# Optimization experiments

Hardware: AMD Instinct MI355X
Metric: run time of the kernel (lower is better)

The kernel has to match this reference:

```python
import jax, jax.numpy as jnp
import numpy as np

B, T, H, LATENT, P = 64, 256, 1024, 256, 128


def _lstm_layer(x, h0, c0, Wih, Whh, bih, bhh):
    """PyTorch-convention single-direction LSTM layer.
    x: (B,T,Din); returns hidden sequence (B,T,H). Gate order: i,f,g,o."""
    # Precompute the input contribution for all timesteps in one big GEMM.
    xg = jnp.einsum('btd,gd->btg', x, Wih) + bih + bhh  # (B,T,4H)

    def step(carry, xg_t):
        h, c = carry
        gates = xg_t + h @ Whh.T  # (B,4H)
        i, f, g, o = jnp.split(gates, 4, axis=-1)
        c = jax.nn.sigmoid(f) * c + jax.nn.sigmoid(i) * jnp.tanh(g)
        h = jax.nn.sigmoid(o) * jnp.tanh(c)
        return (h, c), h

    (_, _), hs = jax.lax.scan(step, (h0, c0), jnp.swapaxes(xg, 0, 1))
    return jnp.swapaxes(hs, 0, 1)  # (B,T,H)


def setup_inputs() -> dict:
    key = jax.random.key(0)
    ks = jax.random.split(key, 8)
    s = lambda fan_in: 1.0 / np.sqrt(fan_in)
    return {
        'z': jax.random.normal(ks[0], (B, LATENT), jnp.float32),
        'target_seq': jax.random.uniform(ks[1], (B, T, P), jnp.float32),
        'fc_init_w': jax.random.normal(ks[2], (H, LATENT), jnp.float32) * s(LATENT),
        'fc_init_b': jnp.zeros((H,), jnp.float32),
        'start_token': jax.random.normal(ks[3], (1, 1, P), jnp.float32) * 0.1,
        'W_ih_l0': jax.random.normal(ks[4], (4 * H, P), jnp.float32) * s(P),
        'W_hh_l0': jax.random.normal(ks[5], (4 * H, H), jnp.float32) * s(H),
        'b_ih_l0': jnp.zeros((4 * H,), jnp.float32),
        'b_hh_l0': jnp.zeros((4 * H,), jnp.float32),
        'W_ih_l1': jax.random.normal(ks[6], (4 * H, H), jnp.float32) * s(H),
        'W_hh_l1': jax.random.normal(ks[7], (4 * H, H), jnp.float32) * s(H),
        'b_ih_l1': jnp.zeros((4 * H,), jnp.float32),
        'b_hh_l1': jnp.zeros((4 * H,), jnp.float32),
        'out_w': jax.random.normal(jax.random.fold_in(key, 99), (P, H), jnp.float32) * s(H),
        'out_b': jnp.zeros((P,), jnp.float32),
    }


def reference(z, target_seq, fc_init_w, fc_init_b, start_token,
              W_ih_l0, W_hh_l0, b_ih_l0, b_hh_l0,
              W_ih_l1, W_hh_l1, b_ih_l1, b_hh_l1,
              out_w, out_b):
    # h0 = fc_init(z), shared across both LSTM layers (repeat over num_layers).
    h0 = z @ fc_init_w.T + fc_init_b  # (B,H)
    c0 = jnp.zeros_like(h0)
    # Full teacher forcing (teacher_forcing_ratio=1.0): input at step t is
    # target_seq[:, t-1]; step 0 uses the learned start token. Dropout is in
    # eval mode (identity).
    x_in = jnp.concatenate(
        [jnp.broadcast_to(start_token, (z.shape[0], 1, start_token.shape[-1])),
         target_seq[:, :-1, :]], axis=1)  # (B,T,P)
    h1 = _lstm_layer(x_in, h0, c0, W_ih_l0, W_hh_l0, b_ih_l0, b_hh_l0)
    h2 = _lstm_layer(h1, h0, c0, W_ih_l1, W_hh_l1, b_ih_l1, b_hh_l1)
    return jax.nn.sigmoid(jnp.einsum('bth,ph->btp', h2, out_w) + out_b)  # (B,T,P)
```

## Files before the change

kernel.cpp:

```cpp
#include <hip/hip_runtime.h>
#include <hip/hip_bf16.h>
#include <stdint.h>

typedef __attribute__((ext_vector_type(8))) short short8;
typedef __attribute__((ext_vector_type(4))) float floatx4;

#define B_ 64
#define T_ 256
#define H_ 1024
#define LATENT_ 256
#define P_ 128
#define BH_ (B_ * H_)
#define MFMA_(a, b, c) __builtin_amdgcn_mfma_f32_16x16x32_bf16(a, b, c, 0, 0, 0)
#define PBI(n, row) (((n) + 4 * (row)) & 31)

#define LDS_TOTAL 65536

#define SLOTS 258
#define ARR(lay, slot, g) \
    ((((size_t)(lay) * SLOTS + (slot)) * 32 + (g)) * 16)
#define FLG(lay, slot, g, r) \
    ((((size_t)(lay) * SLOTS + (slot)) * 32 + 8 + 2 * (g) + (r)) * 16)
#define CNTW (2 * SLOTS * 32 * 16)


__device__ __forceinline__ float sigmoidf_(float x) {
    return 1.0f / (1.0f + __expf(-x));
}
__device__ __forceinline__ float tanh_fast(float x) {
    float e = __expf(2.0f * x);
    return 1.0f - 2.0f / (e + 1.0f);
}

__global__ __launch_bounds__(256) void cvt_f2b(
    const float* __restrict__ src, __hip_bfloat16* __restrict__ dst, int n)
{
    int i = (blockIdx.x * 256 + threadIdx.x) * 4;
    if (i < n) {
        float4 v = *(const float4*)(src + i);
        dst[i + 0] = __float2bfloat16(v.x);
        dst[i + 1] = __float2bfloat16(v.y);
        dst[i + 2] = __float2bfloat16(v.z);
        dst[i + 3] = __float2bfloat16(v.w);
    }
}

__global__ __launch_bounds__(256) void h0_kernel(
    const float* __restrict__ z,
    const float* __restrict__ fw,
    const float* __restrict__ fb,
    __hip_bfloat16* __restrict__ h1dst,
    __hip_bfloat16* __restrict__ h2dst,
    unsigned* __restrict__ cnt)
{
    int idx = blockIdx.x * 256 + threadIdx.x;
    for (int i = idx; i < CNTW; i += 65536) {
        int line = i >> 4;
        int li   = line & 31;
        int slot = (line >> 5) % SLOTS;
        cnt[i] = ((i & 15) == 0 && li >= 8 && li < 24 && slot == 0) ? 1u : 0u;
    }
    int b = idx >> 10, j = idx & 1023;
    const float* zp = z + b * LATENT_;
    const float* wp = fw + j * LATENT_;
    float acc = fb[j];
    for (int k = 0; k < LATENT_; k += 4) {
        float4 zv = *(const float4*)(zp + k);
        float4 wv = *(const float4*)(wp + k);
        acc += zv.x * wv.x + zv.y * wv.y + zv.z * wv.z + zv.w * wv.w;
    }
    __hip_bfloat16 hb = __float2bfloat16(acc);
    int off = ((j >> 3) * 64 + b) * 8 + (j & 7);
    h1dst[off] = hb;
    h2dst[off] = hb;
}

struct PParams {
    const __hip_bfloat16 *tseqb, *stokb;
    const __hip_bfloat16 *Wih0b, *Whh0b, *Wih1b, *Whh1b, *owb;
    const float *bih0, *bhh0, *bih1, *bhh1, *ob;
    __hip_bfloat16 *h1seq;
    __hip_bfloat16 *h2seq;
    float* out;
    unsigned* cnt;
};

__global__ __launch_bounds__(512, 2) void lstm_persistent(PParams p)
{
    extern __shared__ char dynlds[];
    float (*pbuf)[64][32] = (float (*)[64][32])dynlds;

    const int tid  = threadIdx.x;
    const int bid  = blockIdx.x;
    const int wv   = tid >> 6;
    const int l    = tid & 63;
    const int l15  = l & 15;
    const int quad = l >> 4;
    const int ks   = quad * 8;
    const bool isL1 = bid < 128;
    const int colbase = (isL1 ? bid : bid - 128) * 8;
    const int hblk = colbase >> 3;
    const int row0 = ((l15 >> 3)    ) * H_ + colbase + (l15 & 7);
    const int row1 = ((l15 >> 3) + 2) * H_ + colbase + (l15 & 7);

    auto h1slot = [&](int t) { return p.h1seq + (size_t)(t + 1) * BH_; };
    auto h2slot = [&](int t) { return p.h2seq + (size_t)(t + 1) * BH_; };

    auto wspin = [&](int lay, int slot) {
        if (l == 0) {
            const unsigned* cf = p.cnt + FLG(lay, slot, wv, bid & 1);
            while (__hip_atomic_load(cf, __ATOMIC_RELAXED,
                                     __HIP_MEMORY_SCOPE_AGENT) == 0u)
                __builtin_amdgcn_s_sleep(2);
        }
        asm volatile("" ::: "memory");
    };

    short8 bh0r[4], bh1r[4];
    {
        const short* Wh = (const short*)(isL1 ? p.Whh1b : p.Whh0b);
#pragma unroll
        for (int c = 0; c < 4; ++c) {
            int kR = wv * 16 + c * 4 + quad;
            bh0r[c] = *(const short8*)(Wh + (long)row0 * H_ + kR * 8);
            bh1r[c] = *(const short8*)(Wh + (long)row1 * H_ + kR * 8);
        }
    }
    short8 bx0r, bx1r;
    if (!isL1 && wv < 4) {
        const short* Wx = (const short*)p.Wih0b;
        int kcx = wv * 4 + quad;
        bx0r = *(const short8*)(Wx + (long)row0 * P_ + kcx * 8);
        bx1r = *(const short8*)(Wx + (long)row1 * P_ + kcx * 8);
    }

    const int cm  = tid >> 3;
    const int c0  = tid & 7;
    const int cj0 = colbase + c0;
    const float* bi = isL1 ? p.bih1 : p.bih0;
    const float* bh = isL1 ? p.bhh1 : p.bhh0;
    float bs[4];
#pragma unroll
    for (int g = 0; g < 4; ++g)
        bs[g] = bi[g * H_ + cj0] + bh[g * H_ + cj0];
    float creg = 0.0f;

    const int lay = isL1 ? 1 : 0;
    const int agrp = hblk >> 4;

    for (int phase = 0; phase <= T_; ++phase) {
        const bool doGemm = isL1 ? (phase >= 1) : (phase < T_);
        const int t = isL1 ? phase - 1 : phase;
        if (!doGemm) continue;

        floatx4 acc[8] = {};
        if (isL1) {
            wspin(1, phase - 1);
            const short* A2 = (const short*)h2slot(t - 1);
            short8 af2[16];
#pragma unroll
            for (int c = 0; c < 4; ++c)
#pragma unroll
                for (int mt = 0; mt < 4; ++mt) {
                    int kR = wv * 16 + c * 4 + quad;
                    af2[c * 4 + mt] = *(const short8*)(A2 +
                        ((long)(kR * 64 + mt * 16 + l15) << 3));
                }
            wspin(0, phase);
            const short* A1 = (const short*)h1slot(t);
            short8 af1[16];
#pragma unroll
            for (int c = 0; c < 4; ++c)
#pragma unroll
                for (int mt = 0; mt < 4; ++mt) {
                    int kR = wv * 16 + c * 4 + quad;
                    af1[c * 4 + mt] = *(const short8*)(A1 +
                        ((long)(kR * 64 + mt * 16 + l15) << 3));
                }
            const short* w0 = (const short*)p.Wih1b + (long)row0 * H_;
            const short* w1 = (const short*)p.Wih1b + (long)row1 * H_;
            short8 bw0[4], bw1[4];
#pragma unroll
            for (int c = 0; c < 4; ++c) {
                int kR = wv * 16 + c * 4 + quad;
                bw0[c] = *(const short8*)(w0 + kR * 8);
                bw1[c] = *(const short8*)(w1 + kR * 8);
            }
#pragma unroll
            for (int c = 0; c < 4; ++c) {
#pragma unroll
                for (int mt = 0; mt < 4; ++mt) {
                    acc[2 * mt]     = MFMA_(af2[c * 4 + mt], bh0r[c], acc[2 * mt]);
                    acc[2 * mt + 1] = MFMA_(af2[c * 4 + mt], bh1r[c], acc[2 * mt + 1]);
                }
            }
#pragma unroll
            for (int c = 0; c < 4; ++c) {
#pragma unroll
                for (int mt = 0; mt < 4; ++mt) {
                    acc[2 * mt]     = MFMA_(af1[c * 4 + mt], bw0[c], acc[2 * mt]);
                    acc[2 * mt + 1] = MFMA_(af1[c * 4 + mt], bw1[c], acc[2 * mt + 1]);
                }
            }
        } else {
            const short* Ax; long xstr;
            if (t == 0) { Ax = (const short*)p.stokb; xstr = 0; }
            else { Ax = (const short*)p.tseqb + (long)(t - 1) * P_; xstr = (long)T_ * P_; }
            short8 xf[4];
            if (wv < 4) {
#pragma unroll
                for (int mt = 0; mt < 4; ++mt)
                    xf[mt] = *(const short8*)(Ax + (long)(mt * 16 + l15) * xstr + wv * 32 + ks);
            }
            wspin(0, phase);
            const short* Ah = (const short*)h1slot(t - 1);
            short8 af[16];
#pragma unroll
            for (int c = 0; c < 4; ++c)
#pragma unroll
                for (int mt = 0; mt < 4; ++mt) {
                    int kR = wv * 16 + c * 4 + quad;
                    af[c * 4 + mt] = *(const short8*)(Ah +
                        ((long)(kR * 64 + mt * 16 + l15) << 3));
                }
            if (wv < 4) {
#pragma unroll
                for (int mt = 0; mt < 4; ++mt) {
                    acc[2 * mt]     = MFMA_(xf[mt], bx0r, acc[2 * mt]);
                    acc[2 * mt + 1] = MFMA_(xf[mt], bx1r, acc[2 * mt + 1]);
                }
            }
#pragma unroll
            for (int c = 0; c < 4; ++c) {
#pragma unroll
                for (int mt = 0; mt < 4; ++mt) {
                    acc[2 * mt]     = MFMA_(af[c * 4 + mt], bh0r[c], acc[2 * mt]);
                    acc[2 * mt + 1] = MFMA_(af[c * 4 + mt], bh1r[c], acc[2 * mt + 1]);
                }
            }
        }
#pragma unroll
        for (int mt = 0; mt < 4; ++mt)
#pragma unroll
            for (int nt = 0; nt < 2; ++nt)
#pragma unroll
                for (int r = 0; r < 4; ++r) {
                    int row = mt * 16 + quad * 4 + r;
                    pbuf[wv][row][PBI(nt * 16 + l15, row)] = acc[2 * mt + nt][r];
                }
        __syncthreads();

        {
            float v[4];
#pragma unroll
            for (int g = 0; g < 4; ++g) v[g] = bs[g];
#pragma unroll
            for (int w2 = 0; w2 < 8; ++w2)
#pragma unroll
                for (int g = 0; g < 4; ++g)
                    v[g] += pbuf[w2][cm][PBI(8 * g + c0, cm)];
            float cn = sigmoidf_(v[1]) * creg + sigmoidf_(v[0]) * tanh_fast(v[2]);
            float hv = sigmoidf_(v[3]) * tanh_fast(cn);
            creg = cn;
            __hip_bfloat16* hdst = isL1 ? h2slot(t) : h1slot(t);
            __hip_bfloat16 hb = __float2bfloat16(hv);
            unsigned short hu = *(unsigned short*)&hb;
            __hip_atomic_store((unsigned short*)hdst + hblk * 512 + tid, hu,
                               __ATOMIC_RELAXED, __HIP_MEMORY_SCOPE_AGENT);
        }

        __syncthreads();
        if (tid == 0) {
            unsigned old = __hip_atomic_fetch_add(
                p.cnt + ARR(lay, t + 1, agrp), 1u,
                __ATOMIC_RELAXED, __HIP_MEMORY_SCOPE_AGENT);
            if (old == 15u) {
                __hip_atomic_store(p.cnt + FLG(lay, t + 1, agrp, 0), 1u,
                                   __ATOMIC_RELAXED, __HIP_MEMORY_SCOPE_AGENT);
                __hip_atomic_store(p.cnt + FLG(lay, t + 1, agrp, 1), 1u,
                                   __ATOMIC_RELAXED, __HIP_MEMORY_SCOPE_AGENT);
            }
        }
    }

    {
        const int t = bid;
        if (tid == 0) {
            for (int g = 0; g < 8; ++g) {
                const unsigned* cf = p.cnt + FLG(1, t + 1, g, bid & 1);
                while (__hip_atomic_load(cf, __ATOMIC_RELAXED,
                                         __HIP_MEMORY_SCOPE_AGENT) == 0u)
                    __builtin_amdgcn_s_sleep(2);
            }
        }
        asm volatile("" ::: "memory");
        __syncthreads();

        const int nh = wv >> 1, kh = wv & 1;
        const short* A  = (const short*)h2slot(t);
        const short* Wb = (const short*)p.owb;
        floatx4 oacc[8] = {};
        for (int c = 0; c < 16; ++c) {
            int kk = kh * 512 + c * 32 + ks;
            short8 b0 = *(const short8*)(Wb + (long)(nh * 32 + l15) * H_ + kk);
            short8 b1 = *(const short8*)(Wb + (long)(nh * 32 + 16 + l15) * H_ + kk);
#pragma unroll
            for (int mt = 0; mt < 4; ++mt) {
                short8 a = *(const short8*)(A +
                    ((long)((kh * 64 + c * 4 + quad) * 64 + mt * 16 + l15) << 3));
                oacc[2 * mt]     = MFMA_(a, b0, oacc[2 * mt]);
                oacc[2 * mt + 1] = MFMA_(a, b1, oacc[2 * mt + 1]);
            }
        }
#pragma unroll
        for (int mt = 0; mt < 4; ++mt)
#pragma unroll
            for (int nt = 0; nt < 2; ++nt)
#pragma unroll
                for (int r = 0; r < 4; ++r) {
                    int row = mt * 16 + quad * 4 + r;
                    pbuf[wv][row][PBI(nt * 16 + l15, row)] = oacc[2 * mt + nt][r];
                }
        __syncthreads();
        for (int i = tid; i < 64 * 128; i += 512) {
            int m = i >> 7, pp2 = i & 127;
            int nh2 = pp2 >> 5, pc = pp2 & 31;
            float v = pbuf[2 * nh2][m][PBI(pc, m)] + pbuf[2 * nh2 + 1][m][PBI(pc, m)]
                    + p.ob[pp2];
            p.out[(long)m * (T_ * P_) + (long)t * P_ + pp2] = sigmoidf_(v);
        }
    }
}

extern "C" void kernel_launch(void* const* d_in, const int* in_sizes, int n_in,
                              void* d_out, int out_size, void* d_ws, size_t ws_size,
                              hipStream_t stream) {
    const float* z    = (const float*)d_in[0];
    const float* tseq = (const float*)d_in[1];
    const float* fw   = (const float*)d_in[2];
    const float* fb   = (const float*)d_in[3];
    const float* stok = (const float*)d_in[4];
    const float* Wih0 = (const float*)d_in[5];
    const float* Whh0 = (const float*)d_in[6];
    const float* bih0 = (const float*)d_in[7];
    const float* bhh0 = (const float*)d_in[8];
    const float* Wih1 = (const float*)d_in[9];
    const float* Whh1 = (const float*)d_in[10];
    const float* bih1 = (const float*)d_in[11];
    const float* bhh1 = (const float*)d_in[12];
    const float* ow   = (const float*)d_in[13];
    const float* ob   = (const float*)d_in[14];
    float* out = (float*)d_out;

    const size_t FULLH = (size_t)(T_ + 1) * BH_ * 2;
    char* ws = (char*)d_ws;
    size_t off = 0;
    __hip_bfloat16* Wih0b = (__hip_bfloat16*)(ws + off); off += (size_t)4 * H_ * P_ * 2;
    __hip_bfloat16* Whh0b = (__hip_bfloat16*)(ws + off); off += (size_t)4 * H_ * H_ * 2;
    __hip_bfloat16* Wih1b = (__hip_bfloat16*)(ws + off); off += (size_t)4 * H_ * H_ * 2;
    __hip_bfloat16* Whh1b = (__hip_bfloat16*)(ws + off); off += (size_t)4 * H_ * H_ * 2;
    __hip_bfloat16* owb   = (__hip_bfloat16*)(ws + off); off += (size_t)P_ * H_ * 2;
    __hip_bfloat16* tseqb = (__hip_bfloat16*)(ws + off); off += (size_t)B_ * T_ * P_ * 2;
    __hip_bfloat16* stokb = (__hip_bfloat16*)(ws + off); off += 256;
    __hip_bfloat16* h1seq = (__hip_bfloat16*)(ws + off); off += FULLH;
    __hip_bfloat16* h2seq = (__hip_bfloat16*)(ws + off); off += FULLH;
    unsigned* cnt         = (unsigned*)(ws + off);       off += (size_t)CNTW * 4;

    auto cvt = [&](const float* s, __hip_bfloat16* d, int n) {
        hipLaunchKernelGGL(cvt_f2b, dim3((n / 4 + 255) / 256), dim3(256), 0, stream, s, d, n);
    };
    cvt(Wih0, Wih0b, 4 * H_ * P_);
    cvt(Whh0, Whh0b, 4 * H_ * H_);
    cvt(Wih1, Wih1b, 4 * H_ * H_);
    cvt(Whh1, Whh1b, 4 * H_ * H_);
    cvt(ow,   owb,   P_ * H_);
    cvt(tseq, tseqb, B_ * T_ * P_);
    cvt(stok, stokb, P_);

    hipLaunchKernelGGL(h0_kernel, dim3(256), dim3(256), 0, stream,
                       z, fw, fb, h1seq, h2seq, cnt);

    PParams pp;
    pp.tseqb = tseqb; pp.stokb = stokb;
    pp.Wih0b = Wih0b; pp.Whh0b = Whh0b; pp.Wih1b = Wih1b; pp.Whh1b = Whh1b;
    pp.owb = owb;
    pp.bih0 = bih0; pp.bhh0 = bhh0; pp.bih1 = bih1; pp.bhh1 = bhh1; pp.ob = ob;
    pp.h1seq = h1seq; pp.h2seq = h2seq;
    pp.out = out;
    pp.cnt = cnt;

    hipFuncSetAttribute((const void*)lstm_persistent,
                        hipFuncAttributeMaxDynamicSharedMemorySize, LDS_TOTAL);
    void* args[] = { &pp };
    hipLaunchCooperativeKernel((void*)lstm_persistent, dim3(256), dim3(512),
                               args, LDS_TOTAL, stream);
}
```

Before: 1.922 ms.

## Replace atomic counter barrier with per-block byte flags and hoist Wih1 weights

The inter-block step barrier changes from an atomic fetch-add counter plus a flag set by the last arriver to per-block byte markers. Each block writes its own 0xFF byte into two replicated 16-byte lines, and waiters poll those lines with two 64-bit loads until all bytes are set. This takes the serialized atomic RMW and the extra flag-publish hop off the critical path of every timestep. Separately, the layer-1 input weights are loaded once into registers before the loop instead of every phase, which raises register pressure.

```diff
diff --git a/kernel.cpp b/kernel.cpp
--- a/kernel.cpp
+++ b/kernel.cpp
@@ -17,10 +17,8 @@
 #define LDS_TOTAL 65536
 
 #define SLOTS 258
-#define ARR(lay, slot, g) \
-    ((((size_t)(lay) * SLOTS + (slot)) * 32 + (g)) * 16)
-#define FLG(lay, slot, g, r) \
-    ((((size_t)(lay) * SLOTS + (slot)) * 32 + 8 + 2 * (g) + (r)) * 16)
+#define MRK(lay, slot, g, rep) \
+    ((((size_t)(lay) * SLOTS + (slot)) * 32 + 2 * (g) + (rep)) * 16)
 #define CNTW (2 * SLOTS * 32 * 16)
 
 
@@ -56,9 +54,10 @@
     int idx = blockIdx.x * 256 + threadIdx.x;
     for (int i = idx; i < CNTW; i += 65536) {
         int line = i >> 4;
+        int word = i & 15;
         int li   = line & 31;
         int slot = (line >> 5) % SLOTS;
-        cnt[i] = ((i & 15) == 0 && li >= 8 && li < 24 && slot == 0) ? 1u : 0u;
+        cnt[i] = (slot == 0 && li < 16 && word < 4) ? 0xFFFFFFFFu : 0u;
     }
     int b = idx >> 10, j = idx & 1023;
     const float* zp = z + b * LATENT_;
@@ -108,10 +107,16 @@
 
     auto wspin = [&](int lay, int slot) {
         if (l == 0) {
-            const unsigned* cf = p.cnt + FLG(lay, slot, wv, bid & 1);
-            while (__hip_atomic_load(cf, __ATOMIC_RELAXED,
-                                     __HIP_MEMORY_SCOPE_AGENT) == 0u)
+            const unsigned long long* m8 =
+                (const unsigned long long*)(p.cnt + MRK(lay, slot, wv, bid & 1));
+            for (;;) {
+                unsigned long long a = __hip_atomic_load(m8,
+                                        __ATOMIC_RELAXED, __HIP_MEMORY_SCOPE_AGENT);
+                unsigned long long b2 = __hip_atomic_load(m8 + 1,
+                                        __ATOMIC_RELAXED, __HIP_MEMORY_SCOPE_AGENT);
+                if ((a & b2) == ~0ull) break;
                 __builtin_amdgcn_s_sleep(2);
+            }
         }
         asm volatile("" ::: "memory");
     };
@@ -124,6 +129,17 @@
             int kR = wv * 16 + c * 4 + quad;
             bh0r[c] = *(const short8*)(Wh + (long)row0 * H_ + kR * 8);
             bh1r[c] = *(const short8*)(Wh + (long)row1 * H_ + kR * 8);
+        }
+    }
+    short8 bw0r[4], bw1r[4];
+    if (isL1) {
+        const short* w0 = (const short*)p.Wih1b + (long)row0 * H_;
+        const short* w1 = (const short*)p.Wih1b + (long)row1 * H_;
+#pragma unroll
+        for (int c = 0; c < 4; ++c) {
+            int kR = wv * 16 + c * 4 + quad;
+            bw0r[c] = *(const short8*)(w0 + kR * 8);
+            bw1r[c] = *(const short8*)(w1 + kR * 8);
         }
     }
     short8 bx0r, bx1r;
@@ -147,6 +163,7 @@
 
     const int lay = isL1 ? 1 : 0;
     const int agrp = hblk >> 4;
+    const int mbyte = hblk & 15;
 
     for (int phase = 0; phase <= T_; ++phase) {
         const bool doGemm = isL1 ? (phase >= 1) : (phase < T_);
@@ -177,15 +194,6 @@
                     af1[c * 4 + mt] = *(const short8*)(A1 +
                         ((long)(kR * 64 + mt * 16 + l15) << 3));
                 }
-            const short* w0 = (const short*)p.Wih1b + (long)row0 * H_;
-            const short* w1 = (const short*)p.Wih1b + (long)row1 * H_;
-            short8 bw0[4], bw1[4];
-#pragma unroll
-            for (int c = 0; c < 4; ++c) {
-                int kR = wv * 16 + c * 4 + quad;
-                bw0[c] = *(const short8*)(w0 + kR * 8);
-                bw1[c] = *(const short8*)(w1 + kR * 8);
-            }
 #pragma unroll
             for (int c = 0; c < 4; ++c) {
 #pragma unroll
@@ -198,8 +206,8 @@
             for (int c = 0; c < 4; ++c) {
 #pragma unroll
                 for (int mt = 0; mt < 4; ++mt) {
-                    acc[2 * mt]     = MFMA_(af1[c * 4 + mt], bw0[c], acc[2 * mt]);
-                    acc[2 * mt + 1] = MFMA_(af1[c * 4 + mt], bw1[c], acc[2 * mt + 1]);
+                    acc[2 * mt]     = MFMA_(af1[c * 4 + mt], bw0r[c], acc[2 * mt]);
+                    acc[2 * mt + 1] = MFMA_(af1[c * 4 + mt], bw1r[c], acc[2 * mt + 1]);
                 }
             }
         } else {
@@ -271,15 +279,12 @@
 
         __syncthreads();
         if (tid == 0) {
-            unsigned old = __hip_atomic_fetch_add(
-                p.cnt + ARR(lay, t + 1, agrp), 1u,
-                __ATOMIC_RELAXED, __HIP_MEMORY_SCOPE_AGENT);
-            if (old == 15u) {
-                __hip_atomic_store(p.cnt + FLG(lay, t + 1, agrp, 0), 1u,
-                                   __ATOMIC_RELAXED, __HIP_MEMORY_SCOPE_AGENT);
-                __hip_atomic_store(p.cnt + FLG(lay, t + 1, agrp, 1), 1u,
-                                   __ATOMIC_RELAXED, __HIP_MEMORY_SCOPE_AGENT);
-            }
+            unsigned char* m0 = (unsigned char*)(p.cnt + MRK(lay, t + 1, agrp, 0));
+            unsigned char* m1 = (unsigned char*)(p.cnt + MRK(lay, t + 1, agrp, 1));
+            __hip_atomic_store(m0 + mbyte, (unsigned char)0xFF,
+                               __ATOMIC_RELAXED, __HIP_MEMORY_SCOPE_AGENT);
+            __hip_atomic_store(m1 + mbyte, (unsigned char)0xFF,
+                               __ATOMIC_RELAXED, __HIP_MEMORY_SCOPE_AGENT);
         }
     }
 
@@ -287,10 +292,16 @@
         const int t = bid;
         if (tid == 0) {
             for (int g = 0; g < 8; ++g) {
-                const unsigned* cf = p.cnt + FLG(1, t + 1, g, bid & 1);
-                while (__hip_atomic_load(cf, __ATOMIC_RELAXED,
-                                         __HIP_MEMORY_SCOPE_AGENT) == 0u)
+                const unsigned long long* m8 =
+                    (const unsigned long long*)(p.cnt + MRK(1, t + 1, g, bid & 1));
+                for (;;) {
+                    unsigned long long a = __hip_atomic_load(m8,
+                                            __ATOMIC_RELAXED, __HIP_MEMORY_SCOPE_AGENT);
+                    unsigned long long b2 = __hip_atomic_load(m8 + 1,
+                                            __ATOMIC_RELAXED, __HIP_MEMORY_SCOPE_AGENT);
+                    if ((a & b2) == ~0ull) break;
                     __builtin_amdgcn_s_sleep(2);
+                }
             }
         }
         asm volatile("" ::: "memory");
```

Result: slower. 2.434 ms (+26.7%).
